# Performance work log

Measured on AMD Instinct MI355X. Metric: run time of the kernel, lower is better.

The kernel has to match this reference:

```python
import jax, jax.numpy as jnp
import numpy as np

N = 100000
E = 3200000
F_IN = 128


def gcn_conv(x, w, b, src, dst, n):
    """PyG GCNConv: out = D^-1/2 (A + I) D^-1/2 (x @ w) + b.
    src/dst already include self loops."""
    xw = x @ w                                   # [N, F_out]
    ones = jnp.ones(src.shape[0], dtype=xw.dtype)
    deg = jax.ops.segment_sum(ones, dst, num_segments=n)   # in-degree incl. self loop
    dinv = jnp.where(deg > 0, jax.lax.rsqrt(deg), 0.0)
    norm = dinv[src] * dinv[dst]                 # [E+N]
    msg = xw[src] * norm[:, None]                # gather + scale
    out = jax.ops.segment_sum(msg, dst, num_segments=n)
    return out + b


def setup_inputs() -> dict:
    key = jax.random.key(0)
    ks = jax.random.split(key, 10)
    x = jax.random.normal(ks[0], (N, F_IN), dtype=jnp.float32)
    edge_index = jax.random.randint(ks[1], (2, E), 0, N, dtype=jnp.int64)
    # Glorot-ish init for weights
    def lin(k, fi, fo):
        return jax.random.normal(k, (fi, fo), dtype=jnp.float32) / np.sqrt(fi)
    return {
        "x": x,
        "edge_index": edge_index,
        "w1": lin(ks[2], F_IN, 64), "b1": jnp.zeros((64,), jnp.float32),
        "w2": lin(ks[3], 64, 32),   "b2": jnp.zeros((32,), jnp.float32),
        "w3": lin(ks[4], 32, 16),   "b3": jnp.zeros((16,), jnp.float32),
        "w_out": lin(ks[5], 16, 1), "b_out": jnp.zeros((1,), jnp.float32),
    }


def reference(x, edge_index, w1, b1, w2, b2, w3, b3, w_out, b_out):
    n = x.shape[0]
    # add self loops once (PyG adds them inside each GCNConv; same graph => same result)
    loop = jnp.arange(n, dtype=edge_index.dtype)
    src = jnp.concatenate([edge_index[0], loop])
    dst = jnp.concatenate([edge_index[1], loop])
    h = jax.nn.relu(gcn_conv(x, w1, b1, src, dst, n))
    h = jax.nn.relu(gcn_conv(h, w2, b2, src, dst, n))
    h = jax.nn.relu(gcn_conv(h, w3, b3, src, dst, n))
    return h @ w_out + b_out  # [N, 1]
```

## Files before the change

kernel.cpp:

```cpp
#include <hip/hip_runtime.h>
#include <hip/hip_bf16.h>


#define NBUCK 391
#define BSHIFT 8
#define CAP 10240
#define EPB 2048

typedef __attribute__((ext_vector_type(4))) unsigned short ushort4v;
typedef __attribute__((ext_vector_type(8))) unsigned short ushort8v;
typedef __attribute__((ext_vector_type(8))) _Float16 half8;
typedef __attribute__((ext_vector_type(4))) float f32x4;

__device__ __forceinline__ float bf2f(unsigned short u) {
  union { unsigned int i; float f; } v;
  v.i = ((unsigned int)u) << 16;
  return v.f;
}
__device__ __forceinline__ unsigned short f2bf(float f) {
  union { float f; unsigned int i; } v;
  v.f = f;
  unsigned int r = v.i + 0x7FFF + ((v.i >> 16) & 1);
  return (unsigned short)(r >> 16);
}

static __global__ __launch_bounds__(256) void partition_kernel(
    const int* __restrict__ src, const int* __restrict__ dst,
    int* __restrict__ bucket_cnt, int* __restrict__ part, int E) {
  __shared__ int hist[NBUCK];
  __shared__ int bbase[NBUCK];
  const int t = threadIdx.x;
  for (int j = t; j < NBUCK; j += 256) hist[j] = 0;
  __syncthreads();
  const int base = blockIdx.x * EPB + t * 8;
  int ss[8], dd[8];
  if (base + 8 <= E) {
    int4 s0 = *(const int4*)&src[base], s1 = *(const int4*)&src[base + 4];
    int4 d0 = *(const int4*)&dst[base], d1 = *(const int4*)&dst[base + 4];
    ss[0] = s0.x; ss[1] = s0.y; ss[2] = s0.z; ss[3] = s0.w;
    ss[4] = s1.x; ss[5] = s1.y; ss[6] = s1.z; ss[7] = s1.w;
    dd[0] = d0.x; dd[1] = d0.y; dd[2] = d0.z; dd[3] = d0.w;
    dd[4] = d1.x; dd[5] = d1.y; dd[6] = d1.z; dd[7] = d1.w;
  } else {
#pragma unroll
    for (int j = 0; j < 8; ++j) {
      int i = base + j;
      ss[j] = (i < E) ? src[i] : -1;
      dd[j] = (i < E) ? dst[i] : 0;
    }
  }
#pragma unroll
  for (int j = 0; j < 8; ++j)
    if (ss[j] >= 0) atomicAdd(&hist[dd[j] >> BSHIFT], 1);
  __syncthreads();
  for (int j = t; j < NBUCK; j += 256) {
    int h = hist[j];
    bbase[j] = h ? atomicAdd(&bucket_cnt[j], h) : 0;
    hist[j] = 0;
  }
  __syncthreads();
#pragma unroll
  for (int j = 0; j < 8; ++j) {
    if (ss[j] >= 0) {
      int b = dd[j] >> BSHIFT;
      int r = bbase[b] + atomicAdd(&hist[b], 1);
      if (r < CAP) part[(size_t)b * CAP + r] = ((dd[j] & 255) << 17) | ss[j];
    }
  }
}

static __global__ __launch_bounds__(256) void bucket2csr_kernel(
    const int* __restrict__ bucket_cnt, const int* __restrict__ part,
    int* __restrict__ csr_src, int* __restrict__ row_start,
    int* __restrict__ row_end, float* __restrict__ dinv, int n) {
  __shared__ int hist[256];
  __shared__ int cursor[256];
  __shared__ int sdata[256];
  const int b = blockIdx.x;
  const int t = threadIdx.x;
  const int base = b * CAP;
  int cnt = bucket_cnt[b];
  if (cnt > CAP) cnt = CAP;
  hist[t] = 0;
  __syncthreads();
  int i = t * 4;
  for (; i + 4 <= cnt; i += 1024) {
    int4 v = *(const int4*)&part[base + i];
    atomicAdd(&hist[v.x >> 17], 1);
    atomicAdd(&hist[v.y >> 17], 1);
    atomicAdd(&hist[v.z >> 17], 1);
    atomicAdd(&hist[v.w >> 17], 1);
  }
  for (int k = i; k < cnt && k < i + 4; ++k)
    atomicAdd(&hist[part[base + k] >> 17], 1);
  __syncthreads();
  const int v = hist[t];
  const int pd = (v + 7) & ~7;
  sdata[t] = pd;
  __syncthreads();
  int incl = pd;
  for (int off = 1; off < 256; off <<= 1) {
    int y = (t >= off) ? sdata[t - off] : 0;
    __syncthreads();
    incl += y;
    sdata[t] = incl;
    __syncthreads();
  }
  const int excl = incl - pd;
  cursor[t] = excl;
  const int node = b * 256 + t;
  if (node < n) {
    row_start[node] = base + excl;
    row_end[node] = base + excl + pd;
    dinv[node] = rsqrtf((float)(v + 1));
  }
  __syncthreads();
  i = t * 4;
  for (; i + 4 <= cnt; i += 1024) {
    int4 pv = *(const int4*)&part[base + i];
    int p0 = atomicAdd(&cursor[pv.x >> 17], 1);
    csr_src[base + p0] = pv.x & 0x1FFFF;
    int p1 = atomicAdd(&cursor[pv.y >> 17], 1);
    csr_src[base + p1] = pv.y & 0x1FFFF;
    int p2 = atomicAdd(&cursor[pv.z >> 17], 1);
    csr_src[base + p2] = pv.z & 0x1FFFF;
    int p3 = atomicAdd(&cursor[pv.w >> 17], 1);
    csr_src[base + p3] = pv.w & 0x1FFFF;
  }
  for (int k = i; k < cnt && k < i + 4; ++k) {
    int pv = part[base + k];
    int pos = atomicAdd(&cursor[pv >> 17], 1);
    csr_src[base + pos] = pv & 0x1FFFF;
  }
  for (int k = v; k < pd; ++k) csr_src[base + excl + k] = n;
}

static __global__ __launch_bounds__(256) void gemm1_mfma_kernel(
    const float* __restrict__ x, const float* __restrict__ w1,
    const float* __restrict__ dinv, unsigned short* __restrict__ xws, int n) {
  __shared__ _Float16 xa[64 * 128];
  __shared__ _Float16 wt[64 * 128];
  const int t = threadIdx.x;
  const int base = blockIdx.x * 64;
  for (int i = t; i < 64 * 16; i += 256) {
    int r = i >> 4, k8 = i & 15;
    int node = base + r;
    float4 a = {0.f, 0.f, 0.f, 0.f}, b = {0.f, 0.f, 0.f, 0.f};
    if (node < n) {
      a = *(const float4*)&x[(size_t)node * 128 + k8 * 8];
      b = *(const float4*)&x[(size_t)node * 128 + k8 * 8 + 4];
    }
    half8 h = {(_Float16)a.x, (_Float16)a.y, (_Float16)a.z, (_Float16)a.w,
               (_Float16)b.x, (_Float16)b.y, (_Float16)b.z, (_Float16)b.w};
    int byte = (r * 256 + k8 * 16) ^ ((r & 7) << 4);
    *(half8*)((char*)xa + byte) = h;
  }
  for (int i = t; i < 128 * 64; i += 256) {
    int k = i >> 6, o = i & 63;
    _Float16 v = (_Float16)w1[i];
    int byte = (o * 256 + k * 2) ^ ((o & 7) << 4);
    *(_Float16*)((char*)wt + byte) = v;
  }
  __syncthreads();
  const int wv = t >> 6;
  const int lane = t & 63;
  const int m = lane & 15;
  const int kg = lane >> 4;
  const int arow = wv * 16 + m;
  f32x4 acc[4] = {{0.f, 0.f, 0.f, 0.f}, {0.f, 0.f, 0.f, 0.f},
                  {0.f, 0.f, 0.f, 0.f}, {0.f, 0.f, 0.f, 0.f}};
#pragma unroll
  for (int ks = 0; ks < 4; ++ks) {
    int k0 = ks * 32 + kg * 8;
    int abyte = (arow * 256 + k0 * 2) ^ ((arow & 7) << 4);
    half8 af = *(const half8*)((const char*)xa + abyte);
#pragma unroll
    for (int nt = 0; nt < 4; ++nt) {
      int o = nt * 16 + m;
      int bbyte = (o * 256 + k0 * 2) ^ ((o & 7) << 4);
      half8 bf = *(const half8*)((const char*)wt + bbyte);
      acc[nt] = __builtin_amdgcn_mfma_f32_16x16x32_f16(af, bf, acc[nt], 0, 0, 0);
    }
  }
#pragma unroll
  for (int r = 0; r < 4; ++r) {
    int node = base + wv * 16 + kg * 4 + r;
    if (node < n) {
      float dv = dinv[node];
#pragma unroll
      for (int nt = 0; nt < 4; ++nt)
        xws[(size_t)node * 64 + nt * 16 + m] = f2bf(dv * acc[nt][r]);
    }
  }
}

template <int F, int FOUT>
static __global__ __launch_bounds__(256) void agg_gemm_kernel(
    const unsigned short* __restrict__ xws, const int* __restrict__ row_start,
    const int* __restrict__ row_end, const int* __restrict__ csr_src,
    const float* __restrict__ dinv, const float* __restrict__ bias,
    const float* __restrict__ W, unsigned short* __restrict__ xws_next, int n) {
  constexpr int G = F / 8;
  constexpr int NODES = 256 / G;
  constexpr int OUTS = FOUT / G;
  __shared__ float ws[F * FOUT];
  __shared__ float hs[NODES][F + 1];
  const int t = threadIdx.x;
  for (int i = t; i < F * FOUT / 4; i += 256)
    *(float4*)&ws[i * 4] = *(const float4*)&W[i * 4];
  const int nl = t / G;
  const int c = t - nl * G;
  const int node = blockIdx.x * NODES + nl;
  const bool valid = node < n;
  const int safe = valid ? node : 0;
  const int start = valid ? row_start[safe] : 0;
  const int end = valid ? row_end[safe] : 0;
  float acc[8] = {0.f, 0.f, 0.f, 0.f, 0.f, 0.f, 0.f, 0.f};
  for (int e = start; e < end; e += 8) {
    int4 sa = *(const int4*)&csr_src[e];
    int4 sb = *(const int4*)&csr_src[e + 4];
    ushort8v v0 = *(const ushort8v*)&xws[(size_t)sa.x * F + c * 8];
    ushort8v v1 = *(const ushort8v*)&xws[(size_t)sa.y * F + c * 8];
    ushort8v v2 = *(const ushort8v*)&xws[(size_t)sa.z * F + c * 8];
    ushort8v v3 = *(const ushort8v*)&xws[(size_t)sa.w * F + c * 8];
    ushort8v v4 = *(const ushort8v*)&xws[(size_t)sb.x * F + c * 8];
    ushort8v v5 = *(const ushort8v*)&xws[(size_t)sb.y * F + c * 8];
    ushort8v v6 = *(const ushort8v*)&xws[(size_t)sb.z * F + c * 8];
    ushort8v v7 = *(const ushort8v*)&xws[(size_t)sb.w * F + c * 8];
#pragma unroll
    for (int j = 0; j < 8; ++j)
      acc[j] += ((bf2f(v0[j]) + bf2f(v1[j])) + (bf2f(v2[j]) + bf2f(v3[j]))) +
                ((bf2f(v4[j]) + bf2f(v5[j])) + (bf2f(v6[j]) + bf2f(v7[j])));
  }
  ushort8v sv = *(const ushort8v*)&xws[(size_t)safe * F + c * 8];
  const float dv = dinv[safe];
#pragma unroll
  for (int j = 0; j < 8; ++j)
    hs[nl][c * 8 + j] = fmaxf(dv * (acc[j] + bf2f(sv[j])) + bias[c * 8 + j], 0.f);
  __syncthreads();
  float o[OUTS];
#pragma unroll
  for (int j = 0; j < OUTS; ++j) o[j] = 0.f;
#pragma unroll 4
  for (int k = 0; k < F; ++k) {
    float hv = hs[nl][k];
#pragma unroll
    for (int j = 0; j < OUTS; ++j) o[j] += hv * ws[k * FOUT + c * OUTS + j];
  }
  if (valid) {
    ushort4v r = {f2bf(dv * o[0]), f2bf(dv * o[1]), f2bf(dv * o[2]),
                  f2bf(dv * o[3])};
    *(ushort4v*)&xws_next[(size_t)node * FOUT + c * OUTS] = r;
  }
}

static __global__ __launch_bounds__(256) void agg_head_kernel(
    const unsigned short* __restrict__ xws, const int* __restrict__ row_start,
    const int* __restrict__ row_end, const int* __restrict__ csr_src,
    const float* __restrict__ dinv, const float* __restrict__ bias,
    float* __restrict__ out, const float* __restrict__ w_out,
    const float* __restrict__ b_out, int n) {
  constexpr int F = 16, NODES = 128;
  const int t = threadIdx.x;
  const int nl = t >> 1;
  const int c = t & 1;
  const int node = blockIdx.x * NODES + nl;
  if (node >= n) return;
  const int start = row_start[node], end = row_end[node];
  float acc[8] = {0.f, 0.f, 0.f, 0.f, 0.f, 0.f, 0.f, 0.f};
  for (int e = start; e < end; e += 8) {
    int4 sa = *(const int4*)&csr_src[e];
    int4 sb = *(const int4*)&csr_src[e + 4];
    ushort8v v0 = *(const ushort8v*)&xws[(size_t)sa.x * F + c * 8];
    ushort8v v1 = *(const ushort8v*)&xws[(size_t)sa.y * F + c * 8];
    ushort8v v2 = *(const ushort8v*)&xws[(size_t)sa.z * F + c * 8];
    ushort8v v3 = *(const ushort8v*)&xws[(size_t)sa.w * F + c * 8];
    ushort8v v4 = *(const ushort8v*)&xws[(size_t)sb.x * F + c * 8];
    ushort8v v5 = *(const ushort8v*)&xws[(size_t)sb.y * F + c * 8];
    ushort8v v6 = *(const ushort8v*)&xws[(size_t)sb.z * F + c * 8];
    ushort8v v7 = *(const ushort8v*)&xws[(size_t)sb.w * F + c * 8];
#pragma unroll
    for (int j = 0; j < 8; ++j)
      acc[j] += ((bf2f(v0[j]) + bf2f(v1[j])) + (bf2f(v2[j]) + bf2f(v3[j]))) +
                ((bf2f(v4[j]) + bf2f(v5[j])) + (bf2f(v6[j]) + bf2f(v7[j])));
  }
  ushort8v sv = *(const ushort8v*)&xws[(size_t)node * F + c * 8];
  float dv = dinv[node];
  float p = 0.f;
#pragma unroll
  for (int j = 0; j < 8; ++j) {
    float r = fmaxf(dv * (acc[j] + bf2f(sv[j])) + bias[c * 8 + j], 0.f);
    p += r * w_out[c * 8 + j];
  }
  p += __shfl_xor(p, 1);
  if (c == 0) out[node] = p + b_out[0];
}

extern "C" void kernel_launch(void* const* d_in, const int* in_sizes, int n_in,
                              void* d_out, int out_size, void* d_ws, size_t ws_size,
                              hipStream_t stream) {
  const float* x     = (const float*)d_in[0];
  const int*   ei    = (const int*)d_in[1];
  const float* w1    = (const float*)d_in[2];
  const float* b1    = (const float*)d_in[3];
  const float* w2    = (const float*)d_in[4];
  const float* b2    = (const float*)d_in[5];
  const float* w3    = (const float*)d_in[6];
  const float* b3    = (const float*)d_in[7];
  const float* w_out = (const float*)d_in[8];
  const float* b_out = (const float*)d_in[9];
  float* out = (float*)d_out;

  const int n = in_sizes[0] / 128;
  const int E = in_sizes[1] / 2;
  const int* srcA = ei;
  const int* dstA = ei + E;

  char* p = (char*)d_ws;
  auto carve = [&](size_t bytes) {
    void* r = (void*)p;
    p += (bytes + 255) & ~(size_t)255;
    return r;
  };
  const size_t partBytes = (size_t)NBUCK * CAP * 4;
  int*   csr_src    = (int*)carve(partBytes);
  int*   bucket_cnt = (int*)carve((size_t)NBUCK * 4);
  int*   row_start  = (int*)carve((size_t)n * 4);
  int*   row_end    = (int*)carve((size_t)n * 4);
  float* dinv       = (float*)carve((size_t)n * 4);
  char*  regionP    = (char*)carve(partBytes);
  int*   part       = (int*)regionP;
  unsigned short* xws1 = (unsigned short*)regionP;
  unsigned short* xws2 = (unsigned short*)carve((size_t)(n + 1) * 32 * 2);
  unsigned short* xws3 = (unsigned short*)carve((size_t)(n + 1) * 16 * 2);

  hipMemsetAsync(bucket_cnt, 0, (size_t)NBUCK * 4, stream);
  partition_kernel<<<(E + EPB - 1) / EPB, 256, 0, stream>>>(srcA, dstA,
                                                            bucket_cnt, part, E);
  bucket2csr_kernel<<<NBUCK, 256, 0, stream>>>(bucket_cnt, part, csr_src,
                                               row_start, row_end, dinv, n);
  hipMemsetAsync(xws1 + (size_t)n * 64, 0, 64 * 2, stream);
  hipMemsetAsync(xws2 + (size_t)n * 32, 0, 32 * 2, stream);
  hipMemsetAsync(xws3 + (size_t)n * 16, 0, 16 * 2, stream);

  gemm1_mfma_kernel<<<(n + 63) / 64, 256, 0, stream>>>(x, w1, dinv, xws1, n);
  agg_gemm_kernel<64, 32><<<(n + 31) / 32, 256, 0, stream>>>(
      xws1, row_start, row_end, csr_src, dinv, b1, w2, xws2, n);
  agg_gemm_kernel<32, 16><<<(n + 63) / 64, 256, 0, stream>>>(
      xws2, row_start, row_end, csr_src, dinv, b2, w3, xws3, n);
  agg_head_kernel<<<(n + 127) / 128, 256, 0, stream>>>(
      xws3, row_start, row_end, csr_src, dinv, b3, out, w_out, b_out, n);
}
```

Measured before the change: 228.9 us.

## Split neighbor lists across two lane groups and stage buckets in LDS

```diff
diff --git a/kernel.cpp b/kernel.cpp
--- a/kernel.cpp
+++ b/kernel.cpp
@@ -7,6 +7,7 @@
 #define CAP 10240
 #define EPB 2048
 
+typedef __attribute__((ext_vector_type(2))) unsigned short ushort2v;
 typedef __attribute__((ext_vector_type(4))) unsigned short ushort4v;
 typedef __attribute__((ext_vector_type(8))) unsigned short ushort8v;
 typedef __attribute__((ext_vector_type(8))) _Float16 half8;
@@ -73,6 +74,7 @@
     const int* __restrict__ bucket_cnt, const int* __restrict__ part,
     int* __restrict__ csr_src, int* __restrict__ row_start,
     int* __restrict__ row_end, float* __restrict__ dinv, int n) {
+  __shared__ int plds[CAP];
   __shared__ int hist[256];
   __shared__ int cursor[256];
   __shared__ int sdata[256];
@@ -86,13 +88,17 @@
   int i = t * 4;
   for (; i + 4 <= cnt; i += 1024) {
     int4 v = *(const int4*)&part[base + i];
+    *(int4*)&plds[i] = v;
     atomicAdd(&hist[v.x >> 17], 1);
     atomicAdd(&hist[v.y >> 17], 1);
     atomicAdd(&hist[v.z >> 17], 1);
     atomicAdd(&hist[v.w >> 17], 1);
   }
-  for (int k = i; k < cnt && k < i + 4; ++k)
-    atomicAdd(&hist[part[base + k] >> 17], 1);
+  for (int k = i; k < cnt && k < i + 4; ++k) {
+    int pv = part[base + k];
+    plds[k] = pv;
+    atomicAdd(&hist[pv >> 17], 1);
+  }
   __syncthreads();
   const int v = hist[t];
   const int pd = (v + 7) & ~7;
@@ -115,20 +121,8 @@
     dinv[node] = rsqrtf((float)(v + 1));
   }
   __syncthreads();
-  i = t * 4;
-  for (; i + 4 <= cnt; i += 1024) {
-    int4 pv = *(const int4*)&part[base + i];
-    int p0 = atomicAdd(&cursor[pv.x >> 17], 1);
-    csr_src[base + p0] = pv.x & 0x1FFFF;
-    int p1 = atomicAdd(&cursor[pv.y >> 17], 1);
-    csr_src[base + p1] = pv.y & 0x1FFFF;
-    int p2 = atomicAdd(&cursor[pv.z >> 17], 1);
-    csr_src[base + p2] = pv.z & 0x1FFFF;
-    int p3 = atomicAdd(&cursor[pv.w >> 17], 1);
-    csr_src[base + p3] = pv.w & 0x1FFFF;
-  }
-  for (int k = i; k < cnt && k < i + 4; ++k) {
-    int pv = part[base + k];
+  for (int k = t; k < cnt; k += 256) {
+    int pv = plds[k];
     int pos = atomicAdd(&cursor[pv >> 17], 1);
     csr_src[base + pos] = pv & 0x1FFFF;
   }
@@ -200,23 +194,26 @@
     const int* __restrict__ row_end, const int* __restrict__ csr_src,
     const float* __restrict__ dinv, const float* __restrict__ bias,
     const float* __restrict__ W, unsigned short* __restrict__ xws_next, int n) {
-  constexpr int G = F / 8;
-  constexpr int NODES = 256 / G;
-  constexpr int OUTS = FOUT / G;
+  constexpr int GC = F / 8;
+  constexpr int LPN = F / 4;
+  constexpr int NODES = 256 / LPN;
+  constexpr int OUTS = FOUT / LPN;
   __shared__ float ws[F * FOUT];
   __shared__ float hs[NODES][F + 1];
   const int t = threadIdx.x;
   for (int i = t; i < F * FOUT / 4; i += 256)
     *(float4*)&ws[i * 4] = *(const float4*)&W[i * 4];
-  const int nl = t / G;
-  const int c = t - nl * G;
+  const int nl = t / LPN;
+  const int l = t % LPN;
+  const int c = l % GC;
+  const int sub = l / GC;
   const int node = blockIdx.x * NODES + nl;
   const bool valid = node < n;
   const int safe = valid ? node : 0;
   const int start = valid ? row_start[safe] : 0;
   const int end = valid ? row_end[safe] : 0;
   float acc[8] = {0.f, 0.f, 0.f, 0.f, 0.f, 0.f, 0.f, 0.f};
-  for (int e = start; e < end; e += 8) {
+  for (int e = start + sub * 8; e < end; e += 16) {
     int4 sa = *(const int4*)&csr_src[e];
     int4 sb = *(const int4*)&csr_src[e + 4];
     ushort8v v0 = *(const ushort8v*)&xws[(size_t)sa.x * F + c * 8];
@@ -232,11 +229,16 @@
       acc[j] += ((bf2f(v0[j]) + bf2f(v1[j])) + (bf2f(v2[j]) + bf2f(v3[j]))) +
                 ((bf2f(v4[j]) + bf2f(v5[j])) + (bf2f(v6[j]) + bf2f(v7[j])));
   }
-  ushort8v sv = *(const ushort8v*)&xws[(size_t)safe * F + c * 8];
+#pragma unroll
+  for (int j = 0; j < 8; ++j) acc[j] += __shfl_xor(acc[j], GC);
   const float dv = dinv[safe];
-#pragma unroll
-  for (int j = 0; j < 8; ++j)
-    hs[nl][c * 8 + j] = fmaxf(dv * (acc[j] + bf2f(sv[j])) + bias[c * 8 + j], 0.f);
+  if (sub == 0) {
+    ushort8v sv = *(const ushort8v*)&xws[(size_t)safe * F + c * 8];
+#pragma unroll
+    for (int j = 0; j < 8; ++j)
+      hs[nl][c * 8 + j] =
+          fmaxf(dv * (acc[j] + bf2f(sv[j])) + bias[c * 8 + j], 0.f);
+  }
   __syncthreads();
   float o[OUTS];
 #pragma unroll
@@ -245,12 +247,11 @@
   for (int k = 0; k < F; ++k) {
     float hv = hs[nl][k];
 #pragma unroll
-    for (int j = 0; j < OUTS; ++j) o[j] += hv * ws[k * FOUT + c * OUTS + j];
+    for (int j = 0; j < OUTS; ++j) o[j] += hv * ws[k * FOUT + l * OUTS + j];
   }
   if (valid) {
-    ushort4v r = {f2bf(dv * o[0]), f2bf(dv * o[1]), f2bf(dv * o[2]),
-                  f2bf(dv * o[3])};
-    *(ushort4v*)&xws_next[(size_t)node * FOUT + c * OUTS] = r;
+    ushort2v r = {f2bf(dv * o[0]), f2bf(dv * o[1])};
+    *(ushort2v*)&xws_next[(size_t)node * FOUT + l * OUTS] = r;
   }
 }
 
@@ -260,15 +261,17 @@
     const float* __restrict__ dinv, const float* __restrict__ bias,
     float* __restrict__ out, const float* __restrict__ w_out,
     const float* __restrict__ b_out, int n) {
-  constexpr int F = 16, NODES = 128;
-  const int t = threadIdx.x;
-  const int nl = t >> 1;
-  const int c = t & 1;
+  constexpr int F = 16, NODES = 64;
+  const int t = threadIdx.x;
+  const int nl = t >> 2;
+  const int l = t & 3;
+  const int c = l & 1;
+  const int sub = l >> 1;
   const int node = blockIdx.x * NODES + nl;
   if (node >= n) return;
   const int start = row_start[node], end = row_end[node];
   float acc[8] = {0.f, 0.f, 0.f, 0.f, 0.f, 0.f, 0.f, 0.f};
-  for (int e = start; e < end; e += 8) {
+  for (int e = start + sub * 8; e < end; e += 16) {
     int4 sa = *(const int4*)&csr_src[e];
     int4 sb = *(const int4*)&csr_src[e + 4];
     ushort8v v0 = *(const ushort8v*)&xws[(size_t)sa.x * F + c * 8];
@@ -284,6 +287,8 @@
       acc[j] += ((bf2f(v0[j]) + bf2f(v1[j])) + (bf2f(v2[j]) + bf2f(v3[j]))) +
                 ((bf2f(v4[j]) + bf2f(v5[j])) + (bf2f(v6[j]) + bf2f(v7[j])));
   }
+#pragma unroll
+  for (int j = 0; j < 8; ++j) acc[j] += __shfl_xor(acc[j], 2);
   ushort8v sv = *(const ushort8v*)&xws[(size_t)node * F + c * 8];
   float dv = dinv[node];
   float p = 0.f;
@@ -293,7 +298,7 @@
     p += r * w_out[c * 8 + j];
   }
   p += __shfl_xor(p, 1);
-  if (c == 0) out[node] = p + b_out[0];
+  if (l == 0) out[node] = p + b_out[0];
 }
 
 extern "C" void kernel_launch(void* const* d_in, const int* in_sizes, int n_in,
@@ -344,10 +349,10 @@
   hipMemsetAsync(xws3 + (size_t)n * 16, 0, 16 * 2, stream);
 
   gemm1_mfma_kernel<<<(n + 63) / 64, 256, 0, stream>>>(x, w1, dinv, xws1, n);
-  agg_gemm_kernel<64, 32><<<(n + 31) / 32, 256, 0, stream>>>(
+  agg_gemm_kernel<64, 32><<<(n + 15) / 16, 256, 0, stream>>>(
       xws1, row_start, row_end, csr_src, dinv, b1, w2, xws2, n);
-  agg_gemm_kernel<32, 16><<<(n + 63) / 64, 256, 0, stream>>>(
+  agg_gemm_kernel<32, 16><<<(n + 31) / 32, 256, 0, stream>>>(
       xws2, row_start, row_end, csr_src, dinv, b2, w3, xws3, n);
-  agg_head_kernel<<<(n + 127) / 128, 256, 0, stream>>>(
+  agg_head_kernel<<<(n + 63) / 64, 256, 0, stream>>>(
       xws3, row_start, row_end, csr_src, dinv, b3, out, w_out, b_out, n);
 }
```

After: 215.5 us. -5.8%, faster.
